# Optimization experiments

Hardware: AMD Instinct MI355X
Metric: run time of the kernel (lower is better)

Reference implementation:

```python
import jax, jax.numpy as jnp
import numpy as np

B, NPM, NVM, D, H, DFF, NL = 4, 200, 1500, 512, 8, 2048, 3
PM_COV, VM_COV = 16, 16
S = NPM + NVM + 2
DH = D // H


def _ln(x, s, b):
    mu = jnp.mean(x, -1, keepdims=True)
    var = jnp.mean((x - mu) ** 2, -1, keepdims=True)
    return (x - mu) / jnp.sqrt(var + 1e-5) * s + b


def _forward(vm_states, num_step_states, pm_states, rel, pad_vm,
             pm_W, pm_b, vm_W, vm_b, ln1_s, ln1_b, Wqkv, bqkv, Wo, bo,
             ln2_s, ln2_b, W1, b1, W2, b2, out_W, out_b, cr_W, cr_b):
    b = vm_states.shape[0]
    tok0 = jnp.tile(num_step_states, (1, 1, D))                      # [b,1,D]
    pm_enc = pm_states @ pm_W + pm_b                                 # [b,NPM,D]
    vm_enc = vm_states @ vm_W + vm_b                                 # [b,NVM,D]
    critic_tok = -jnp.ones((b, 1, D), vm_states.dtype)
    x = jnp.concatenate([tok0, pm_enc, vm_enc, critic_tok], axis=1)  # [b,S,D]

    # relation-based local mask: interior token i may attend j iff rel[i]==rel[j]
    inner = rel[:, :, None] != rel[:, None, :]                       # [b,S-2,S-2]
    local = jnp.zeros((b, S, S), bool).at[:, 1:-1, 1:-1].set(inner)
    pad = jnp.zeros((b, S), bool).at[:, 1 + NPM:-1].set(pad_vm)
    mask = local | pad[:, None, :]                                   # True = blocked

    neg = jnp.asarray(-1e9, x.dtype)
    scale = DH ** -0.5
    for i in range(NL):  # pre-norm transformer blocks (dropout=0, eval)
        h = _ln(x, ln1_s[i], ln1_b[i])
        qkv = h @ Wqkv[i] + bqkv[i]
        q, k, v = jnp.split(qkv, 3, axis=-1)
        q = q.reshape(b, S, H, DH)
        k = k.reshape(b, S, H, DH)
        v = v.reshape(b, S, H, DH)
        scores = jnp.einsum('bqhd,bkhd->bhqk', q, k) * scale
        scores = jnp.where(mask[:, None], neg, scores)
        attn = jax.nn.softmax(scores, axis=-1)
        o = jnp.einsum('bhqk,bkhd->bqhd', attn, v).reshape(b, S, D)
        x = x + o @ Wo[i] + bo[i]
        h2 = _ln(x, ln2_s[i], ln2_b[i])
        x = x + jax.nn.gelu(h2 @ W1[i] + b1[i], approximate=False) @ W2[i] + b2[i]

    score = (x[:, 1 + NPM:-1] @ out_W + out_b)[..., 0]               # [b,NVM]
    critic = x[:, -1] @ cr_W + cr_b                                  # [b,1]
    return score, critic


def setup_inputs() -> dict:
    key = jax.random.key(0)
    ks = jax.random.split(key, 16)
    sc = 0.02
    return {
        'vm_states': jax.random.normal(ks[0], (B, NVM, VM_COV), jnp.float32),
        'num_step_states': jax.random.uniform(ks[1], (B, 1, 1), jnp.float32),
        'pm_states': jax.random.normal(ks[2], (B, NPM, PM_COV), jnp.float32),
        'vm_pm_relation': jax.random.randint(ks[3], (B, NPM + NVM, 1), 0, NPM),
        'num_vms_mask': jnp.zeros((B, NVM), bool),
        'pm_W': sc * jax.random.normal(ks[4], (PM_COV, D)), 'pm_b': jnp.zeros((D,)),
        'vm_W': sc * jax.random.normal(ks[5], (VM_COV, D)), 'vm_b': jnp.zeros((D,)),
        'ln1_s': jnp.ones((NL, D)), 'ln1_b': jnp.zeros((NL, D)),
        'Wqkv': sc * jax.random.normal(ks[6], (NL, D, 3 * D)), 'bqkv': jnp.zeros((NL, 3 * D)),
        'Wo': sc * jax.random.normal(ks[7], (NL, D, D)), 'bo': jnp.zeros((NL, D)),
        'ln2_s': jnp.ones((NL, D)), 'ln2_b': jnp.zeros((NL, D)),
        'W1': sc * jax.random.normal(ks[8], (NL, D, DFF)), 'b1': jnp.zeros((NL, DFF)),
        'W2': sc * jax.random.normal(ks[9], (NL, DFF, D)), 'b2': jnp.zeros((NL, D)),
        'out_W': sc * jax.random.normal(ks[10], (D, 1)), 'out_b': jnp.zeros((1,)),
        'cr_W': sc * jax.random.normal(ks[11], (D, 1)), 'cr_b': jnp.zeros((1,)),
    }


def reference(vm_states, num_step_states, pm_states, vm_pm_relation, num_vms_mask,
              pm_W, pm_b, vm_W, vm_b, ln1_s, ln1_b, Wqkv, bqkv, Wo, bo,
              ln2_s, ln2_b, W1, b1, W2, b2, out_W, out_b, cr_W, cr_b):
    rel = vm_pm_relation[:, :, 0]
    return _forward(vm_states, num_step_states, pm_states, rel, num_vms_mask,
                    pm_W, pm_b, vm_W, vm_b, ln1_s, ln1_b, Wqkv, bqkv, Wo, bo,
                    ln2_s, ln2_b, W1, b1, W2, b2, out_W, out_b, cr_W, cr_b)
```

## Files before the change

### kernel.cpp

```cpp
#include <hip/hip_runtime.h>
#include <hip/hip_bf16.h>
#include <math.h>

typedef __hip_bfloat16 bf16;
typedef __attribute__((ext_vector_type(8))) short short8;
typedef __attribute__((ext_vector_type(4))) float f32x4;

constexpr int Bc   = 4;
constexpr int NPM  = 200;
constexpr int NVM  = 1500;
constexpr int Dc   = 512;
constexpr int Hc   = 8;
constexpr int DFF  = 2048;
constexpr int NLc  = 3;
constexpr int Sc   = NPM + NVM + 2;
constexpr int Mrows = Bc * Sc;
constexpr int DH   = Dc / Hc;
constexpr int NTOK = NPM + NVM;
constexpr int NCH  = (Sc + 63) / 64;
constexpr int NQKV = 3 * Dc;
constexpr int GMPAD = 112;

__device__ __forceinline__ float toF(float v) { return v; }
__device__ __forceinline__ float toF(bf16 v)  { return __bfloat162float(v); }
__device__ __forceinline__ void  stO(float* p, float v) { *p = v; }
__device__ __forceinline__ void  stO(bf16*  p, float v) { *p = __float2bfloat16(v); }

__device__ __forceinline__ void gl16(const bf16* g, bf16* l) {
    __builtin_amdgcn_global_load_lds(
        (const __attribute__((address_space(1))) unsigned int*)g,
        (__attribute__((address_space(3))) unsigned int*)l, 16, 0, 0);
}

__device__ __forceinline__ void ld8(const bf16* p, float* out) {
    uint4 u = *(const uint4*)p;
    const unsigned short* s = (const unsigned short*)&u;
    #pragma unroll
    for (int e = 0; e < 8; e++) out[e] = __uint_as_float(((unsigned)s[e]) << 16);
}

__device__ __forceinline__ float ldDual(const void* p, int f, size_t i) {
    if (f) return __bfloat162float(((const bf16*)p)[i]);
    return ((const float*)p)[i];
}

__global__ void detect_kernel(const void* __restrict__ ones_arr, int* __restrict__ flag) {
    unsigned int w = *(const unsigned int*)ones_arr;
    *flag = (w == 0x3F803F80u) ? 1 : 0;
}

__global__ __launch_bounds__(256) void build_bins(
    const int* __restrict__ rel, const unsigned char* __restrict__ pad,
    int* __restrict__ binStart, int* __restrict__ binLen, int* __restrict__ keyList)
{
    int b = blockIdx.x;
    __shared__ int cnt[NPM];
    __shared__ int cur[NPM];
    int tid = threadIdx.x;
    for (int i = tid; i < NPM; i += 256) cnt[i] = 0;
    __syncthreads();
    for (int i = tid; i < NTOK; i += 256) {
        int r = rel[b * NTOK + i];
        bool ok = (r >= 0 && r < NPM);
        if (i >= NPM && pad[b * NVM + (i - NPM)] != 0) ok = false;
        if (ok) atomicAdd(&cnt[r], 1);
    }
    __syncthreads();
    if (tid == 0) {
        int acc = 0;
        for (int g = 0; g < NPM; g++) {
            cur[g] = acc; binStart[b * NPM + g] = acc; binLen[b * NPM + g] = cnt[g];
            acc += cnt[g];
        }
    }
    __syncthreads();
    for (int i = tid; i < NTOK; i += 256) {
        int r = rel[b * NTOK + i];
        bool ok = (r >= 0 && r < NPM);
        if (i >= NPM && pad[b * NVM + (i - NPM)] != 0) ok = false;
        if (ok) {
            int pos = atomicAdd(&cur[r], 1);
            keyList[b * NTOK + pos] = 1 + i;
        }
    }
}

__global__ __launch_bounds__(256) void transposeAll(
    const void* __restrict__ Wq, size_t oq, const void* __restrict__ Wo, size_t oo,
    const void* __restrict__ W1, size_t o1, const void* __restrict__ W2, size_t o2,
    const int* __restrict__ flag,
    bf16* __restrict__ Tq, bf16* __restrict__ To,
    bf16* __restrict__ T1, bf16* __restrict__ T2)
{
    int id = blockIdx.x;
    const void* in; size_t woff; bf16* out; int R, Cn, local;
    if (id < 768)       { in = Wq; woff = oq; out = Tq; R = 512;  Cn = 1536; local = id; }
    else if (id < 1024) { in = Wo; woff = oo; out = To; R = 512;  Cn = 512;  local = id - 768; }
    else if (id < 2048) { in = W1; woff = o1; out = T1; R = 512;  Cn = 2048; local = id - 1024; }
    else                { in = W2; woff = o2; out = T2; R = 2048; Cn = 512;  local = id - 2048; }
    int nbx = Cn >> 5;
    int bx = (local % nbx) * 32, by = (local / nbx) * 32;
    __shared__ float tile[32][33];
    int tx = threadIdx.x & 31, ty = threadIdx.x >> 5;
    int f = *flag;
    #pragma unroll
    for (int i = 0; i < 32; i += 8)
        tile[ty + i][tx] = ldDual(in, f, woff + (size_t)(by + ty + i) * Cn + bx + tx);
    __syncthreads();
    #pragma unroll
    for (int i = 0; i < 32; i += 8)
        out[(size_t)(bx + ty + i) * R + by + tx] = __float2bfloat16(tile[tx][ty + i]);
}

__global__ __launch_bounds__(256) void embed_kernel(
    const void* __restrict__ vm_states, const void* __restrict__ num_step,
    const void* __restrict__ pm_states,
    const void* __restrict__ pm_W, const void* __restrict__ pm_b,
    const void* __restrict__ vm_W, const void* __restrict__ vm_b,
    const int* __restrict__ flag, float* __restrict__ x)
{
    int s = blockIdx.x;
    int b = blockIdx.y;
    int tid = threadIdx.x;
    int f = *flag;
    float* xr = x + ((size_t)b * Sc + s) * Dc;
    if (s == 0) {
        float v = ldDual(num_step, f, b);
        xr[tid] = v; xr[tid + 256] = v;
        return;
    }
    if (s == Sc - 1) {
        xr[tid] = -1.0f; xr[tid + 256] = -1.0f;
        return;
    }
    const void *st, *W, *bias;
    size_t base;
    if (s <= NPM) { st = pm_states; base = ((size_t)b * NPM + (s - 1)) * 16; W = pm_W; bias = pm_b; }
    else          { st = vm_states; base = ((size_t)b * NVM + (s - 1 - NPM)) * 16; W = vm_W; bias = vm_b; }
    __shared__ float sv[16];
    if (tid < 16) sv[tid] = ldDual(st, f, base + tid);
    __syncthreads();
    #pragma unroll
    for (int j = 0; j < 2; j++) {
        int d = tid + j * 256;
        float a = ldDual(bias, f, d);
        #pragma unroll
        for (int c = 0; c < 16; c++)
            a += sv[c] * ldDual(W, f, (size_t)c * Dc + d);
        xr[d] = a;
    }
}

__global__ __launch_bounds__(256) void ln_kernel(
    const float* __restrict__ x, bf16* __restrict__ h,
    const void* __restrict__ sg, const void* __restrict__ bg,
    size_t goff, const int* __restrict__ flag)
{
    int row = blockIdx.x;
    int tid = threadIdx.x;
    int f = *flag;
    const float* xr = x + (size_t)row * Dc;
    float v0 = xr[tid], v1 = xr[tid + 256];
    __shared__ float red[4];
    int lane = tid & 63, wave = tid >> 6;

    float t = v0 + v1;
    #pragma unroll
    for (int off = 32; off > 0; off >>= 1) t += __shfl_down(t, off);
    if (lane == 0) red[wave] = t;
    __syncthreads();
    float mean = (red[0] + red[1] + red[2] + red[3]) * (1.0f / Dc);
    __syncthreads();

    float d0 = v0 - mean, d1 = v1 - mean;
    t = d0 * d0 + d1 * d1;
    #pragma unroll
    for (int off = 32; off > 0; off >>= 1) t += __shfl_down(t, off);
    if (lane == 0) red[wave] = t;
    __syncthreads();
    float var = (red[0] + red[1] + red[2] + red[3]) * (1.0f / Dc);
    float rstd = rsqrtf(var + 1e-5f);

    bf16* hr = h + (size_t)row * Dc;
    hr[tid]       = __float2bfloat16(d0 * rstd * ldDual(sg, f, goff + tid)       + ldDual(bg, f, goff + tid));
    hr[tid + 256] = __float2bfloat16(d1 * rstd * ldDual(sg, f, goff + tid + 256) + ldDual(bg, f, goff + tid + 256));
}

template<int ACT, int OUTMODE, typename OT>
__global__ __launch_bounds__(256) void gemm_mfma(
    const bf16* __restrict__ A, const bf16* __restrict__ Wt,
    const void* __restrict__ biasp, size_t boff, const int* __restrict__ flag,
    OT* __restrict__ C, int M, int N, int K, int Ksplit)
{
    __shared__ __align__(16) bf16 smem[8192];
    bf16* As = smem;
    bf16* Ws = smem + 4096;
    int tid  = threadIdx.x;
    int wave = tid >> 6, lane = tid & 63;

    unsigned nXB  = gridDim.x;
    unsigned flat = blockIdx.y * nXB + blockIdx.x;
    unsigned xcd  = flat & 7;
    unsigned slot = flat >> 3;
    unsigned yb   = xcd * (gridDim.y >> 3) + slot / nXB;
    unsigned xb   = slot - (slot / nXB) * nXB;
    int bm = yb * 64, bn = xb * 64;
    if (bm >= M) return;

    int wm = (wave & 1) * 32, wn = (wave >> 1) * 32;
    int quad = lane >> 4, l16 = lane & 15;
    int lr = lane >> 3;
    int lc = (((lane & 7) ^ lr) & 7) * 8;

    int kBeg = blockIdx.z * Ksplit;
    int kEnd = kBeg + Ksplit;

    f32x4 acc[2][2] = {};

    for (int k0 = kBeg; k0 < kEnd; k0 += 64) {
        #pragma unroll
        for (int c2 = 0; c2 < 2; c2++) {
            int rb = c2 * 32 + wave * 8;
            int ga = bm + rb + lr;
            if (ga >= M) ga = M - 1;
            gl16(A + (size_t)ga * K + k0 + lc, As + rb * 64);
        }
        #pragma unroll
        for (int c2 = 0; c2 < 2; c2++) {
            int rb = c2 * 32 + wave * 8;
            gl16(Wt + (size_t)(bn + rb + lr) * K + k0 + lc, Ws + rb * 64);
        }
        __syncthreads();
        #pragma unroll
        for (int ks = 0; ks < 2; ks++) {
            int sw = (((ks * 4 + quad) ^ (l16 & 7)) & 7) * 8;
            short8 a[2], b[2];
            #pragma unroll
            for (int mi = 0; mi < 2; mi++)
                a[mi] = *(const short8*)(As + (wm + mi * 16 + l16) * 64 + sw);
            #pragma unroll
            for (int nj = 0; nj < 2; nj++)
                b[nj] = *(const short8*)(Ws + (wn + nj * 16 + l16) * 64 + sw);
            #pragma unroll
            for (int mi = 0; mi < 2; mi++)
                #pragma unroll
                for (int nj = 0; nj < 2; nj++)
                    acc[mi][nj] = __builtin_amdgcn_mfma_f32_16x16x32_bf16(
                        a[mi], b[nj], acc[mi][nj], 0, 0, 0);
        }
        __syncthreads();
    }

    int f = *flag;
    bool addBias = (blockIdx.z == 0);

    if (OUTMODE == 0) {
        bf16* Cs = smem;
        #pragma unroll
        for (int mi = 0; mi < 2; mi++) {
            #pragma unroll
            for (int nj = 0; nj < 2; nj++) {
                #pragma unroll
                for (int r = 0; r < 4; r++) {
                    int row = wm + mi * 16 + quad * 4 + r;
                    int col = wn + nj * 16 + l16;
                    float c = acc[mi][nj][r];
                    if (addBias) c += ldDual(biasp, f, boff + bn + col);
                    if (ACT == 1) c = 0.5f * c * (1.0f + erff(c * 0.70710678118654752f));
                    if (ACT == 2 && ((bn + col) >> 9) == 0) c *= 0.125f;
                    Cs[row * 68 + col] = __float2bfloat16(c);
                }
            }
        }
        __syncthreads();
        #pragma unroll
        for (int p = 0; p < 2; p++) {
            int row = p * 32 + (tid >> 3);
            int col = (tid & 7) * 8;
            int gm = bm + row;
            if (gm < M)
                *(uint4*)&((bf16*)C)[(size_t)gm * N + bn + col] = *(const uint4*)&Cs[row * 68 + col];
        }
    } else {
        #pragma unroll
        for (int mi = 0; mi < 2; mi++) {
            #pragma unroll
            for (int nj = 0; nj < 2; nj++) {
                #pragma unroll
                for (int r = 0; r < 4; r++) {
                    int m = bm + wm + mi * 16 + quad * 4 + r;
                    int n = bn + wn + nj * 16 + l16;
                    if (m >= M) continue;
                    float c = acc[mi][nj][r];
                    if (addBias) c += ldDual(biasp, f, boff + n);
                    if (ACT == 1) c = 0.5f * c * (1.0f + erff(c * 0.70710678118654752f));
                    if (OUTMODE == 2) {
                        atomicAdd((float*)&C[(size_t)m * N + n], c);
                    } else {
                        float c2 = c + toF(C[(size_t)m * N + n]);
                        stO(&C[(size_t)m * N + n], c2);
                    }
                }
            }
        }
    }
}

__global__ __launch_bounds__(256) void attn_sparse(
    const bf16* __restrict__ qkv, const int* __restrict__ rel,
    const int* __restrict__ binStart, const int* __restrict__ binLen,
    const int* __restrict__ keyList, bf16* __restrict__ o)
{
    int b = blockIdx.y;
    int wave = threadIdx.x >> 6, lane = threadIdx.x & 63;
    int s = 1 + blockIdx.x * 4 + wave;
    int g = rel[b * NTOK + s - 1];
    int start = 0, len = 0;
    if (g >= 0 && g < NPM) { start = binStart[b * NPM + g]; len = binLen[b * NPM + g]; }
    const int* kl = keyList + b * NTOK + start;

    const bf16* base = qkv + (size_t)b * Sc * NQKV;
    float q8[8];
    ld8(base + (size_t)s * NQKV + lane * 8, q8);
    float od[8] = {};
    float l = 0.f;
    int total = len + 2;
    for (int jj = 0; jj < total; jj += 4) {
        int kk[4]; float msk4[4];
        #pragma unroll
        for (int u = 0; u < 4; u++) {
            int j = jj + u;
            bool v = (j < total);
            int k = 0;
            if (v) k = (j == 0) ? 0 : (j == 1 ? Sc - 1 : kl[j - 2]);
            kk[u] = k; msk4[u] = v ? 1.0f : 0.0f;
        }
        float k8[4][8], v8[4][8];
        #pragma unroll
        for (int u = 0; u < 4; u++) {
            const bf16* kr = base + (size_t)kk[u] * NQKV + lane * 8;
            ld8(kr + 512, k8[u]);
            ld8(kr + 1024, v8[u]);
        }
        float t[4];
        #pragma unroll
        for (int u = 0; u < 4; u++) {
            float d0 = q8[0] * k8[u][0] + q8[1] * k8[u][1] + q8[2] * k8[u][2] + q8[3] * k8[u][3];
            float d1 = q8[4] * k8[u][4] + q8[5] * k8[u][5] + q8[6] * k8[u][6] + q8[7] * k8[u][7];
            t[u] = d0 + d1;
        }
        #pragma unroll
        for (int m2 = 1; m2 <= 4; m2 <<= 1) {
            #pragma unroll
            for (int u = 0; u < 4; u++) t[u] += __shfl_xor(t[u], m2);
        }
        #pragma unroll
        for (int u = 0; u < 4; u++) {
            float p = msk4[u] * __expf(t[u]);
            l += p;
            #pragma unroll
            for (int e = 0; e < 8; e++) od[e] += p * v8[u][e];
        }
    }
    float inv = 1.0f / l;
    unsigned short r8[8];
    #pragma unroll
    for (int e = 0; e < 8; e++) {
        bf16 v = __float2bfloat16(od[e] * inv);
        r8[e] = *(unsigned short*)&v;
    }
    *(uint4*)&o[((size_t)b * Sc + s) * Dc + lane * 8] = *(uint4*)r8;
}

__global__ __launch_bounds__(256) void attn_dense_part(
    const bf16* __restrict__ qkv, const unsigned char* __restrict__ pad,
    float* __restrict__ pOd, float* __restrict__ pL)
{
    int c = blockIdx.x;
    int q2 = blockIdx.y;
    int b = blockIdx.z;
    int q = q2 ? (Sc - 1) : 0;
    int wave = threadIdx.x >> 6, lane = threadIdx.x & 63;
    const bf16* base = qkv + (size_t)b * Sc * NQKV;
    float q8[8];
    ld8(base + (size_t)q * NQKV + lane * 8, q8);
    float od[8] = {};
    float l = 0.f;
    #pragma unroll 2
    for (int i = 0; i < 16; i++) {
        int k = c * 64 + wave * 16 + i;
        if (k >= Sc) break;
        bool masked = (k >= 1 + NPM && k <= NPM + NVM) && (pad[b * NVM + k - 1 - NPM] != 0);
        if (!masked) {
            const bf16* kr = base + (size_t)k * NQKV + lane * 8;
            float k8[8], v8[8];
            ld8(kr + 512, k8);
            ld8(kr + 1024, v8);
            float t = q8[0]*k8[0] + q8[1]*k8[1] + q8[2]*k8[2] + q8[3]*k8[3]
                    + q8[4]*k8[4] + q8[5]*k8[5] + q8[6]*k8[6] + q8[7]*k8[7];
            #pragma unroll
            for (int m2 = 1; m2 <= 4; m2 <<= 1) t += __shfl_xor(t, m2);
            float p = __expf(t);
            l += p;
            #pragma unroll
            for (int e = 0; e < 8; e++) od[e] += p * v8[e];
        }
    }
    __shared__ float ol[4][512];
    __shared__ float ls[4][8];
    #pragma unroll
    for (int e = 0; e < 8; e++) ol[wave][lane * 8 + e] = od[e];
    if ((lane & 7) == 0) ls[wave][lane >> 3] = l;
    __syncthreads();
    int slot = (b * 2 + q2) * NCH + c;
    int tid = threadIdx.x;
    #pragma unroll
    for (int rep = 0; rep < 2; rep++) {
        int d = tid + rep * 256;
        pOd[(size_t)slot * 512 + d] = ol[0][d] + ol[1][d] + ol[2][d] + ol[3][d];
    }
    if (tid < 8) pL[slot * 8 + tid] = ls[0][tid] + ls[1][tid] + ls[2][tid] + ls[3][tid];
}

__global__ __launch_bounds__(512) void attn_dense_red(
    const float* __restrict__ pOd, const float* __restrict__ pL,
    bf16* __restrict__ o)
{
    int q2 = blockIdx.x;
    int b = blockIdx.y;
    int q = q2 ? (Sc - 1) : 0;
    int d = threadIdx.x;
    int base = (b * 2 + q2) * NCH;
    float od = 0.f, l = 0.f;
    int h = d >> 6;
    for (int c = 0; c < NCH; c++) {
        od += pOd[(size_t)(base + c) * 512 + d];
        l  += pL[(base + c) * 8 + h];
    }
    o[((size_t)b * Sc + q) * Dc + d] = __float2bfloat16(od / l);
}

__global__ __launch_bounds__(64) void out_kernel(
    const float* __restrict__ x,
    const void* __restrict__ out_W, const void* __restrict__ out_b,
    const void* __restrict__ cr_W,  const void* __restrict__ cr_b,
    const int* __restrict__ flag, void* __restrict__ out)
{
    int gid = blockIdx.x;
    int b = gid / (NVM + 1), r = gid % (NVM + 1);
    int f = *flag;
    const float* xr;
    const void* w;
    float bias;
    size_t oidx;
    if (r < NVM) {
        xr = x + ((size_t)b * Sc + 1 + NPM + r) * Dc;
        w = out_W; bias = ldDual(out_b, f, 0);
        oidx = (size_t)b * NVM + r;
    } else {
        xr = x + ((size_t)b * Sc + Sc - 1) * Dc;
        w = cr_W; bias = ldDual(cr_b, f, 0);
        oidx = (size_t)Bc * NVM + b;
    }
    int lane = threadIdx.x;
    float t = 0.0f;
    #pragma unroll
    for (int i = 0; i < 8; i++) {
        int d = lane + i * 64;
        t += xr[d] * ldDual(w, f, d);
    }
    #pragma unroll
    for (int off = 32; off > 0; off >>= 1) t += __shfl_down(t, off);
    if (lane == 0) {
        float r2 = t + bias;
        if (f) ((bf16*)out)[oidx]  = __float2bfloat16(r2);
        else   ((float*)out)[oidx] = r2;
    }
}

extern "C" void kernel_launch(void* const* d_in, const int* in_sizes, int n_in,
                              void* d_out, int out_size, void* d_ws, size_t ws_size,
                              hipStream_t stream)
{
    const void* vm_states = d_in[0];
    const void* num_step  = d_in[1];
    const void* pm_states = d_in[2];
    const int*  rel       = (const int*)d_in[3];
    const unsigned char* pad = (const unsigned char*)d_in[4];
    const void* pm_W  = d_in[5];
    const void* pm_b  = d_in[6];
    const void* vm_W  = d_in[7];
    const void* vm_b  = d_in[8];
    const void* ln1_s = d_in[9];
    const void* ln1_b = d_in[10];
    const void* Wqkv  = d_in[11];
    const void* bqkv  = d_in[12];
    const void* Wo    = d_in[13];
    const void* bo    = d_in[14];
    const void* ln2_s = d_in[15];
    const void* ln2_b = d_in[16];
    const void* W1    = d_in[17];
    const void* b1    = d_in[18];
    const void* W2    = d_in[19];
    const void* b2    = d_in[20];
    const void* out_W = d_in[21];
    const void* out_b = d_in[22];
    const void* cr_W  = d_in[23];
    const void* cr_b  = d_in[24];

    int* flag = (int*)d_ws;
    const size_t xsz = (size_t)Mrows * Dc;
    float* x   = (float*)((char*)d_ws + 64);
    bf16*  hb  = (bf16*)(x + xsz);
    bf16*  big = hb + xsz;
    bf16*  Wt  = big + (size_t)Mrows * DFF;
    bf16*  WtQ = Wt;
    bf16*  WtO = Wt + 786432;
    bf16*  Wt1 = Wt + 1048576;
    bf16*  Wt2 = Wt + 2097152;
    int*   bins = (int*)(Wt + 3145728);
    int*   binStart = bins;
    int*   binLen   = bins + Bc * NPM;
    int*   keyList  = bins + 2 * Bc * NPM;
    float* pOd = (float*)(keyList + Bc * NTOK);
    float* pL  = pOd + (size_t)Bc * 2 * NCH * 512;

    detect_kernel<<<1, 1, 0, stream>>>(ln1_s, flag);
    build_bins<<<Bc, 256, 0, stream>>>(rel, pad, binStart, binLen, keyList);

    dim3 egrid(Sc, Bc);
    embed_kernel<<<egrid, 256, 0, stream>>>(vm_states, num_step, pm_states,
                                            pm_W, pm_b, vm_W, vm_b, flag, x);

    for (int l = 0; l < NLc; l++) {
        size_t oD   = (size_t)l * Dc;
        size_t oQKV = (size_t)l * Dc * 3 * Dc;
        size_t obQ  = (size_t)l * 3 * Dc;
        size_t oWo  = (size_t)l * Dc * Dc;
        size_t oW1  = (size_t)l * Dc * DFF;
        size_t ob1  = (size_t)l * DFF;
        size_t oW2  = (size_t)l * DFF * Dc;

        transposeAll<<<3072, 256, 0, stream>>>(Wqkv, oQKV, Wo, oWo, W1, oW1, W2, oW2,
                                               flag, WtQ, WtO, Wt1, Wt2);

        ln_kernel<<<Mrows, 256, 0, stream>>>(x, hb, ln1_s, ln1_b, oD, flag);

        gemm_mfma<2, 0, bf16><<<dim3(24, GMPAD), 256, 0, stream>>>(
            hb, WtQ, bqkv, obQ, flag, big, Mrows, NQKV, Dc, Dc);

        attn_sparse<<<dim3(425, Bc), 256, 0, stream>>>(
            big, rel, binStart, binLen, keyList, hb);
        attn_dense_part<<<dim3(NCH, 2, Bc), 256, 0, stream>>>(big, pad, pOd, pL);
        attn_dense_red<<<dim3(2, Bc), 512, 0, stream>>>(pOd, pL, hb);

        gemm_mfma<0, 2, float><<<dim3(8, GMPAD, 2), 256, 0, stream>>>(
            hb, WtO, bo, oD, flag, x, Mrows, Dc, Dc, Dc / 2);

        ln_kernel<<<Mrows, 256, 0, stream>>>(x, hb, ln2_s, ln2_b, oD, flag);

        gemm_mfma<1, 0, bf16><<<dim3(32, GMPAD), 256, 0, stream>>>(
            hb, Wt1, b1, ob1, flag, big, Mrows, DFF, Dc, Dc);

        gemm_mfma<0, 2, float><<<dim3(8, GMPAD, 2), 256, 0, stream>>>(
            big, Wt2, b2, oD, flag, x, Mrows, Dc, DFF, DFF / 2);
    }

    out_kernel<<<Bc * (NVM + 1), 64, 0, stream>>>(x, out_W, out_b, cr_W, cr_b,
                                                  flag, d_out);
}
```

Before: 733.6 us.

## Replace GEMM with weight-resident LDS tiles and direct-from-global A fragments

Replaces the 64x64 double-operand LDS tiled GEMM with a kernel that loads a whole BN x KP weight slab into LDS once, then streams A fragments straight from global memory into MFMA operands without a K-loop barrier. Row tiles grow to 128 per block and the tile shapes are set per GEMM (the W2 GEMM uses 32x1024 slabs with a 2-way K split). The aim is to remove the per-K-step __syncthreads and the A staging through LDS. The costs are large LDS footprints, which limit occupancy, uncoalesced-ish direct A loads, and bf16 stores that no longer go through LDS staging.

```diff
diff --git a/kernel.cpp b/kernel.cpp
--- a/kernel.cpp
+++ b/kernel.cpp
@@ -19,7 +19,7 @@
 constexpr int NTOK = NPM + NVM;
 constexpr int NCH  = (Sc + 63) / 64;
 constexpr int NQKV = 3 * Dc;
-constexpr int GMPAD = 112;
+constexpr int NMT  = (Mrows + 127) / 128;
 
 __device__ __forceinline__ float toF(float v) { return v; }
 __device__ __forceinline__ float toF(bf16 v)  { return __bfloat162float(v); }
@@ -186,120 +186,82 @@
     hr[tid + 256] = __float2bfloat16(d1 * rstd * ldDual(sg, f, goff + tid + 256) + ldDual(bg, f, goff + tid + 256));
 }
 
-template<int ACT, int OUTMODE, typename OT>
-__global__ __launch_bounds__(256) void gemm_mfma(
+template<int BN, int KP, int ACT, int OUTMODE, typename OT>
+__global__ __launch_bounds__(256) void gemm_bres(
     const bf16* __restrict__ A, const bf16* __restrict__ Wt,
     const void* __restrict__ biasp, size_t boff, const int* __restrict__ flag,
-    OT* __restrict__ C, int M, int N, int K, int Ksplit)
-{
-    __shared__ __align__(16) bf16 smem[8192];
-    bf16* As = smem;
-    bf16* Ws = smem + 4096;
+    OT* __restrict__ C, int M, int N, int K)
+{
+    __shared__ __align__(16) bf16 Bs[BN * KP];
+    constexpr int NJ  = BN / 16;
+    constexpr int CPR = KP / 8;
+    constexpr int CSH = (KP == 256) ? 5 : (KP == 512 ? 6 : 7);
+
     int tid  = threadIdx.x;
     int wave = tid >> 6, lane = tid & 63;
-
-    unsigned nXB  = gridDim.x;
-    unsigned flat = blockIdx.y * nXB + blockIdx.x;
-    unsigned xcd  = flat & 7;
-    unsigned slot = flat >> 3;
-    unsigned yb   = xcd * (gridDim.y >> 3) + slot / nXB;
-    unsigned xb   = slot - (slot / nXB) * nXB;
-    int bm = yb * 64, bn = xb * 64;
-    if (bm >= M) return;
-
-    int wm = (wave & 1) * 32, wn = (wave >> 1) * 32;
     int quad = lane >> 4, l16 = lane & 15;
-    int lr = lane >> 3;
-    int lc = (((lane & 7) ^ lr) & 7) * 8;
-
-    int kBeg = blockIdx.z * Ksplit;
-    int kEnd = kBeg + Ksplit;
-
-    f32x4 acc[2][2] = {};
-
-    for (int k0 = kBeg; k0 < kEnd; k0 += 64) {
-        #pragma unroll
-        for (int c2 = 0; c2 < 2; c2++) {
-            int rb = c2 * 32 + wave * 8;
-            int ga = bm + rb + lr;
-            if (ga >= M) ga = M - 1;
-            gl16(A + (size_t)ga * K + k0 + lc, As + rb * 64);
-        }
-        #pragma unroll
-        for (int c2 = 0; c2 < 2; c2++) {
-            int rb = c2 * 32 + wave * 8;
-            gl16(Wt + (size_t)(bn + rb + lr) * K + k0 + lc, Ws + rb * 64);
-        }
-        __syncthreads();
-        #pragma unroll
-        for (int ks = 0; ks < 2; ks++) {
-            int sw = (((ks * 4 + quad) ^ (l16 & 7)) & 7) * 8;
-            short8 a[2], b[2];
-            #pragma unroll
-            for (int mi = 0; mi < 2; mi++)
-                a[mi] = *(const short8*)(As + (wm + mi * 16 + l16) * 64 + sw);
-            #pragma unroll
-            for (int nj = 0; nj < 2; nj++)
-                b[nj] = *(const short8*)(Ws + (wn + nj * 16 + l16) * 64 + sw);
-            #pragma unroll
-            for (int mi = 0; mi < 2; mi++)
-                #pragma unroll
-                for (int nj = 0; nj < 2; nj++)
-                    acc[mi][nj] = __builtin_amdgcn_mfma_f32_16x16x32_bf16(
-                        a[mi], b[nj], acc[mi][nj], 0, 0, 0);
-        }
-        __syncthreads();
+
+    int bn    = blockIdx.x * BN;
+    int m0    = blockIdx.y * 128;
+    int kbase = blockIdx.z * KP;
+
+    constexpr int TOT = (BN * KP) / 512;
+    #pragma unroll
+    for (int j = wave; j < TOT; j += 4) {
+        int c   = j * 64 + lane;
+        int row = c >> CSH;
+        int qp  = c & (CPR - 1);
+        int ql  = qp ^ (row & 7);
+        gl16(Wt + (size_t)(bn + row) * K + kbase + ql * 8, Bs + j * 512);
+    }
+    __syncthreads();
+
+    int wrow = m0 + wave * 32;
+    int ga0 = wrow + l16;      if (ga0 >= M) ga0 = M - 1;
+    int ga1 = wrow + 16 + l16; if (ga1 >= M) ga1 = M - 1;
+    const bf16* a0p = A + (size_t)ga0 * K + kbase + quad * 8;
+    const bf16* a1p = A + (size_t)ga1 * K + kbase + quad * 8;
+
+    f32x4 acc[2][NJ] = {};
+
+    #pragma unroll 4
+    for (int ks = 0; ks < KP / 32; ks++) {
+        short8 a0 = *(const short8*)(a0p + ks * 32);
+        short8 a1 = *(const short8*)(a1p + ks * 32);
+        short8 bfr[NJ];
+        #pragma unroll
+        for (int nj = 0; nj < NJ; nj++) {
+            int n  = nj * 16 + l16;
+            int ph = (ks * 4 + quad) ^ (n & 7);
+            bfr[nj] = *(const short8*)(Bs + n * KP + ph * 8);
+        }
+        #pragma unroll
+        for (int nj = 0; nj < NJ; nj++) {
+            acc[0][nj] = __builtin_amdgcn_mfma_f32_16x16x32_bf16(a0, bfr[nj], acc[0][nj], 0, 0, 0);
+            acc[1][nj] = __builtin_amdgcn_mfma_f32_16x16x32_bf16(a1, bfr[nj], acc[1][nj], 0, 0, 0);
+        }
     }
 
     int f = *flag;
     bool addBias = (blockIdx.z == 0);
 
-    if (OUTMODE == 0) {
-        bf16* Cs = smem;
-        #pragma unroll
-        for (int mi = 0; mi < 2; mi++) {
+    #pragma unroll
+    for (int mi = 0; mi < 2; mi++) {
+        #pragma unroll
+        for (int nj = 0; nj < NJ; nj++) {
             #pragma unroll
-            for (int nj = 0; nj < 2; nj++) {
-                #pragma unroll
-                for (int r = 0; r < 4; r++) {
-                    int row = wm + mi * 16 + quad * 4 + r;
-                    int col = wn + nj * 16 + l16;
-                    float c = acc[mi][nj][r];
-                    if (addBias) c += ldDual(biasp, f, boff + bn + col);
-                    if (ACT == 1) c = 0.5f * c * (1.0f + erff(c * 0.70710678118654752f));
-                    if (ACT == 2 && ((bn + col) >> 9) == 0) c *= 0.125f;
-                    Cs[row * 68 + col] = __float2bfloat16(c);
-                }
-            }
-        }
-        __syncthreads();
-        #pragma unroll
-        for (int p = 0; p < 2; p++) {
-            int row = p * 32 + (tid >> 3);
-            int col = (tid & 7) * 8;
-            int gm = bm + row;
-            if (gm < M)
-                *(uint4*)&((bf16*)C)[(size_t)gm * N + bn + col] = *(const uint4*)&Cs[row * 68 + col];
-        }
-    } else {
-        #pragma unroll
-        for (int mi = 0; mi < 2; mi++) {
-            #pragma unroll
-            for (int nj = 0; nj < 2; nj++) {
-                #pragma unroll
-                for (int r = 0; r < 4; r++) {
-                    int m = bm + wm + mi * 16 + quad * 4 + r;
-                    int n = bn + wn + nj * 16 + l16;
-                    if (m >= M) continue;
-                    float c = acc[mi][nj][r];
-                    if (addBias) c += ldDual(biasp, f, boff + n);
-                    if (ACT == 1) c = 0.5f * c * (1.0f + erff(c * 0.70710678118654752f));
-                    if (OUTMODE == 2) {
-                        atomicAdd((float*)&C[(size_t)m * N + n], c);
-                    } else {
-                        float c2 = c + toF(C[(size_t)m * N + n]);
-                        stO(&C[(size_t)m * N + n], c2);
-                    }
+            for (int r = 0; r < 4; r++) {
+                int row = wrow + mi * 16 + quad * 4 + r;
+                if (row >= M) continue;
+                int n = bn + nj * 16 + l16;
+                float c = acc[mi][nj][r];
+                if (addBias) c += ldDual(biasp, f, boff + n);
+                if (ACT == 1) c = 0.5f * c * (1.0f + erff(c * 0.70710678118654752f));
+                if (ACT == 2 && ((bn + nj * 16) >> 9) == 0) c *= 0.125f;
+                if (OUTMODE == 2) {
+                    atomicAdd((float*)&C[(size_t)row * N + n], c);
+                } else {
+                    stO(&C[(size_t)row * N + n], c);
                 }
             }
         }
@@ -546,24 +508,24 @@
 
         ln_kernel<<<Mrows, 256, 0, stream>>>(x, hb, ln1_s, ln1_b, oD, flag);
 
-        gemm_mfma<2, 0, bf16><<<dim3(24, GMPAD), 256, 0, stream>>>(
-            hb, WtQ, bqkv, obQ, flag, big, Mrows, NQKV, Dc, Dc);
+        gemm_bres<64, 512, 2, 0, bf16><<<dim3(24, NMT, 1), 256, 0, stream>>>(
+            hb, WtQ, bqkv, obQ, flag, big, Mrows, NQKV, Dc);
 
         attn_sparse<<<dim3(425, Bc), 256, 0, stream>>>(
             big, rel, binStart, binLen, keyList, hb);
         attn_dense_part<<<dim3(NCH, 2, Bc), 256, 0, stream>>>(big, pad, pOd, pL);
         attn_dense_red<<<dim3(2, Bc), 512, 0, stream>>>(pOd, pL, hb);
 
-        gemm_mfma<0, 2, float><<<dim3(8, GMPAD, 2), 256, 0, stream>>>(
-            hb, WtO, bo, oD, flag, x, Mrows, Dc, Dc, Dc / 2);
+        gemm_bres<64, 256, 0, 2, float><<<dim3(8, NMT, 2), 256, 0, stream>>>(
+            hb, WtO, bo, oD, flag, x, Mrows, Dc, Dc);
 
         ln_kernel<<<Mrows, 256, 0, stream>>>(x, hb, ln2_s, ln2_b, oD, flag);
 
-        gemm_mfma<1, 0, bf16><<<dim3(32, GMPAD), 256, 0, stream>>>(
-            hb, Wt1, b1, ob1, flag, big, Mrows, DFF, Dc, Dc);
-
-        gemm_mfma<0, 2, float><<<dim3(8, GMPAD, 2), 256, 0, stream>>>(
-            big, Wt2, b2, oD, flag, x, Mrows, Dc, DFF, DFF / 2);
+        gemm_bres<64, 512, 1, 0, bf16><<<dim3(32, NMT, 1), 256, 0, stream>>>(
+            hb, Wt1, b1, ob1, flag, big, Mrows, DFF, Dc);
+
+        gemm_bres<32, 1024, 0, 2, float><<<dim3(16, NMT, 2), 256, 0, stream>>>(
+            big, Wt2, b2, oD, flag, x, Mrows, Dc, DFF);
     }
 
     out_kernel<<<Bc * (NVM + 1), 64, 0, stream>>>(x, out_W, out_b, cr_W, cr_b,
```

New measurement: 971.9 us. 1.32x slower.

## Double-buffer GEMM shared-memory tiles with async global loads ahead

Applied to the files above, without the earlier changes.

The MFMA GEMM now keeps two shared-memory stages and issues the global-to-LDS loads for tile t+2 while computing tile t. Explicit vmcnt waits and raw s_barrier calls replace the per-iteration __syncthreads pair, so memory latency can overlap with MFMA work. This doubles LDS use per block to 32 KB, which may lower occupancy. It also relies on exact vmcnt accounting of the four loads per stage, which could break if gl16 is ever changed.

```diff
diff --git a/kernel.cpp b/kernel.cpp
--- a/kernel.cpp
+++ b/kernel.cpp
@@ -192,9 +192,7 @@
     const void* __restrict__ biasp, size_t boff, const int* __restrict__ flag,
     OT* __restrict__ C, int M, int N, int K, int Ksplit)
 {
-    __shared__ __align__(16) bf16 smem[8192];
-    bf16* As = smem;
-    bf16* Ws = smem + 4096;
+    __shared__ __align__(16) bf16 smem[16384];
     int tid  = threadIdx.x;
     int wave = tid >> 6, lane = tid & 63;
 
@@ -213,24 +211,35 @@
     int lc = (((lane & 7) ^ lr) & 7) * 8;
 
     int kBeg = blockIdx.z * Ksplit;
-    int kEnd = kBeg + Ksplit;
+    int nt   = Ksplit >> 6;
+
+    int ga0 = bm + 0  + wave * 8 + lr; if (ga0 >= M) ga0 = M - 1;
+    int ga1 = bm + 32 + wave * 8 + lr; if (ga1 >= M) ga1 = M - 1;
 
     f32x4 acc[2][2] = {};
 
-    for (int k0 = kBeg; k0 < kEnd; k0 += 64) {
-        #pragma unroll
-        for (int c2 = 0; c2 < 2; c2++) {
-            int rb = c2 * 32 + wave * 8;
-            int ga = bm + rb + lr;
-            if (ga >= M) ga = M - 1;
-            gl16(A + (size_t)ga * K + k0 + lc, As + rb * 64);
-        }
-        #pragma unroll
-        for (int c2 = 0; c2 < 2; c2++) {
-            int rb = c2 * 32 + wave * 8;
-            gl16(Wt + (size_t)(bn + rb + lr) * K + k0 + lc, Ws + rb * 64);
-        }
-        __syncthreads();
+    auto STAGE = [&](int t) {
+        bf16* As = smem + (t & 1) * 8192;
+        bf16* Ws = As + 4096;
+        int k0 = kBeg + t * 64;
+        gl16(A + (size_t)ga0 * K + k0 + lc, As + (wave * 8) * 64);
+        gl16(A + (size_t)ga1 * K + k0 + lc, As + (32 + wave * 8) * 64);
+        gl16(Wt + (size_t)(bn + 0  + wave * 8 + lr) * K + k0 + lc, Ws + (wave * 8) * 64);
+        gl16(Wt + (size_t)(bn + 32 + wave * 8 + lr) * K + k0 + lc, Ws + (32 + wave * 8) * 64);
+    };
+
+    STAGE(0);
+    STAGE(1);
+
+    for (int t = 0; t < nt; ++t) {
+        if (t + 1 < nt) asm volatile("s_waitcnt vmcnt(4)" ::: "memory");
+        else            asm volatile("s_waitcnt vmcnt(0)" ::: "memory");
+        __builtin_amdgcn_sched_barrier(0);
+        __builtin_amdgcn_s_barrier();
+        __builtin_amdgcn_sched_barrier(0);
+
+        bf16* As = smem + (t & 1) * 8192;
+        bf16* Ws = As + 4096;
         #pragma unroll
         for (int ks = 0; ks < 2; ks++) {
             int sw = (((ks * 4 + quad) ^ (l16 & 7)) & 7) * 8;
@@ -248,13 +257,18 @@
                     acc[mi][nj] = __builtin_amdgcn_mfma_f32_16x16x32_bf16(
                         a[mi], b[nj], acc[mi][nj], 0, 0, 0);
         }
-        __syncthreads();
+
+        __builtin_amdgcn_sched_barrier(0);
+        __builtin_amdgcn_s_barrier();
+        __builtin_amdgcn_sched_barrier(0);
+        if (t + 2 < nt) STAGE(t + 2);
     }
 
     int f = *flag;
     bool addBias = (blockIdx.z == 0);
 
     if (OUTMODE == 0) {
+        __syncthreads();
         bf16* Cs = smem;
         #pragma unroll
         for (int mi = 0; mi < 2; mi++) {
```

After: 751.5 us. +2.4%, slower.
